# Kernel optimization log

Hardware: AMD Instinct MI355X
Metric: run time of the kernel (lower is better)

The kernel has to match this reference:

```python
import jax, jax.numpy as jnp
import numpy as np

N, D = 8192, 1024


def setup_inputs() -> dict:
    key = jax.random.key(0)
    k1, k2, k3 = jax.random.split(key, 3)
    f_1 = jax.random.normal(k1, (N, D), dtype=jnp.float32)
    f_2 = jax.random.normal(k2, (N, D), dtype=jnp.float32)
    f_3 = jax.random.normal(k3, (N, D), dtype=jnp.float32)
    return {"f_1": f_1, "f_2": f_2, "f_3": f_3, "batch": 3}


def _svdvals(x):
    # torch.svd computes full U, S, V; only singular values are consumed.
    return jnp.linalg.svd(x, compute_uv=False)


def reference(f_1, f_2, f_3, batch):
    if batch == 2:
        s_1 = _svdvals(f_1)
        if f_2.shape[0] == 0:
            return s_1[0] ** 2
        s_2 = _svdvals(f_2)
        return s_1.mean() + s_2.mean()
    elif batch == 3:
        s_1 = _svdvals(f_1)
        s_2 = _svdvals(f_2)
        s_3 = _svdvals(f_3)
        return s_1[0] ** 2 + 0.5 * (s_2[0] ** 2 + s_3[0] ** 2)
```

## Files before the change

kernel.cpp:

```cpp
#include <hip/hip_runtime.h>


#define DIM 1024
#define NROW 8192
#define MSZ (DIM*DIM)
#define NS 6

typedef __attribute__((ext_vector_type(8))) short short8;
typedef __attribute__((ext_vector_type(4))) float f32x4;

__device__ inline float bf2f(unsigned short u) {
    union { unsigned i; float f; } x; x.i = ((unsigned)u) << 16; return x.f;
}
__device__ inline unsigned short f2bf(float f) {
    union { float f; unsigned i; } x; x.f = f;
    unsigned r = x.i + 0x7FFFu + ((x.i >> 16) & 1u);
    return (unsigned short)(r >> 16);
}
__device__ inline void gload16(const void* g, void* l) {
    __builtin_amdgcn_global_load_lds(
        (const __attribute__((address_space(1))) unsigned int*)g,
        (__attribute__((address_space(3))) unsigned int*)l, 16, 0, 0);
}

__global__ __launch_bounds__(256)
void tconv_k(const float* __restrict__ f0, const float* __restrict__ f1,
             const float* __restrict__ f2, unsigned short* __restrict__ ft) {
    const int m = blockIdx.z;
    const float* f = (m == 0) ? f0 : (m == 1 ? f1 : f2);
    unsigned short* o = ft + (size_t)m * DIM * NROW;
    __shared__ float T[64][68];
    const int c0 = blockIdx.x * 64, r0 = blockIdx.y * 64;
    const int tid = threadIdx.x;
    const int cx = (tid & 15) * 4, ry = tid >> 4;
#pragma unroll
    for (int i = 0; i < 4; ++i) {
        int r = ry + i * 16;
        float4 v = *(const float4*)&f[(size_t)(r0 + r) * DIM + c0 + cx];
        T[cx + 0][r] = v.x;
        T[cx + 1][r] = v.y;
        T[cx + 2][r] = v.z;
        T[cx + 3][r] = v.w;
    }
    __syncthreads();
#pragma unroll
    for (int i = 0; i < 4; ++i) {
        int c = ry + i * 16;
        float4 g = *(const float4*)&T[c][cx];
        ushort4 u;
        u.x = f2bf(g.x); u.y = f2bf(g.y); u.z = f2bf(g.z); u.w = f2bf(g.w);
        *(ushort4*)&o[(size_t)(c0 + c) * NROW + r0 + cx] = u;
    }
}

__global__ __launch_bounds__(256)
void syrk_sk(const unsigned short* __restrict__ src, size_t mstride, int KF,
             float* __restrict__ Gp) {
    const int m = blockIdx.z;
    const unsigned short* S = src + (size_t)m * mstride;
    int idx = blockIdx.x, ti = 0;
    while (idx >= 8 - ti) { idx -= 8 - ti; ++ti; }
    const int tj = ti + idx;
    const int i0 = ti * 128, j0 = tj * 128;
    float* G = Gp + ((size_t)m * 36 + blockIdx.x) * 16384;
    const int Kc = KF / gridDim.y;
    const int k0b = blockIdx.y * Kc;

    __shared__ unsigned short As[2 * 128 * 32];
    __shared__ unsigned short Bs[2 * 128 * 32];

    const int tid = threadIdx.x, w = tid >> 6, lane = tid & 63;
    const int wi = w >> 1, wj = w & 1;

    f32x4 acc[4][4];
#pragma unroll
    for (int a = 0; a < 4; ++a)
#pragma unroll
        for (int b = 0; b < 4; ++b) acc[a][b] = (f32x4){0.f, 0.f, 0.f, 0.f};

    const int lr = lane >> 2;
    const int ksw = (((lane & 3) ^ ((lane >> 4) & 3)) * 8);
    const int fr = lane & 15;
    const int slot = (((lane >> 4) ^ ((fr >> 2) & 3)) * 8);

    for (int k0 = k0b; k0 < k0b + Kc; k0 += 64) {
#pragma unroll
        for (int h = 0; h < 2; ++h)
#pragma unroll
            for (int q = 0; q < 2; ++q) {
                int rr = w * 32 + q * 16;
                gload16(S + (size_t)(i0 + rr + lr) * KF + k0 + h * 32 + ksw,
                        &As[h * 4096 + rr * 32]);
                gload16(S + (size_t)(j0 + rr + lr) * KF + k0 + h * 32 + ksw,
                        &Bs[h * 4096 + rr * 32]);
            }
        __syncthreads();
#pragma unroll
        for (int h = 0; h < 2; ++h) {
            short8 af[4], bfv[4];
#pragma unroll
            for (int a = 0; a < 4; ++a)
                af[a] = *(const short8*)&As[h * 4096 + (wi * 64 + a * 16 + fr) * 32 + slot];
#pragma unroll
            for (int b = 0; b < 4; ++b)
                bfv[b] = *(const short8*)&Bs[h * 4096 + (wj * 64 + b * 16 + fr) * 32 + slot];
#pragma unroll
            for (int a = 0; a < 4; ++a)
#pragma unroll
                for (int b = 0; b < 4; ++b)
                    acc[a][b] = __builtin_amdgcn_mfma_f32_16x16x32_bf16(
                        af[a], bfv[b], acc[a][b], 0, 0, 0);
        }
        __syncthreads();
    }

    const int qr = (lane >> 4) * 4, cn = lane & 15;
#pragma unroll
    for (int a = 0; a < 4; ++a)
#pragma unroll
        for (int b = 0; b < 4; ++b) {
            int cl = wj * 64 + b * 16 + cn;
#pragma unroll
            for (int reg = 0; reg < 4; ++reg) {
                int rl = wi * 64 + a * 16 + qr + reg;
                atomicAdd(&G[rl * 128 + cl], acc[a][b][reg]);
            }
        }
}

__global__ __launch_bounds__(256)
void convert_k(const float* __restrict__ Gp, float* __restrict__ trout,
               unsigned short* __restrict__ dst) {
    const int m = blockIdx.z;
    int idx = blockIdx.x, ti = 0;
    while (idx >= 8 - ti) { idx -= 8 - ti; ++ti; }
    const int tj = ti + idx;
    const int i0 = ti * 128, j0 = tj * 128;
    const float* G = Gp + ((size_t)m * 36 + blockIdx.x) * 16384;
    unsigned short* D = dst + (size_t)m * MSZ;
    __shared__ unsigned short T[128][136];
    const int tid = threadIdx.x;
    const int cx = (tid & 31) * 4, ry = tid >> 5;
    float dtr = 0.f;
#pragma unroll 4
    for (int t = 0; t < 16; ++t) {
        int r = ry + t * 8;
        float4 g = *(const float4*)&G[r * 128 + cx];
        ushort4 o;
        o.x = f2bf(g.x); o.y = f2bf(g.y); o.z = f2bf(g.z); o.w = f2bf(g.w);
        *(ushort4*)&D[(size_t)(i0 + r) * DIM + j0 + cx] = o;
        int rs = r ^ (cx & 124);
        T[cx + 0][rs] = o.x; T[cx + 1][rs] = o.y;
        T[cx + 2][rs] = o.z; T[cx + 3][rs] = o.w;
        if (ti == tj) {
            int d = r - cx;
            if (d >= 0 && d < 4)
                dtr += (d == 0 ? g.x : d == 1 ? g.y : d == 2 ? g.z : g.w);
        }
    }
    if (ti == tj) atomicAdd(&trout[m], dtr);
    if (ti != tj) {
        __syncthreads();
#pragma unroll 4
        for (int t = 0; t < 16; ++t) {
            int p = ry + t * 8;
            int qs = cx ^ (p & 124);
            ushort4 o = *(const ushort4*)&T[p][qs];
            *(ushort4*)&D[(size_t)(j0 + p) * DIM + i0 + cx] = o;
        }
    }
}

__global__ __launch_bounds__(256)
void sq_k(const unsigned short* __restrict__ src, const float* __restrict__ trin,
          float* __restrict__ trout, unsigned short* __restrict__ dst) {
    const int m = blockIdx.z;
    const unsigned short* S = src + (size_t)m * MSZ;
    unsigned short* D = dst + (size_t)m * MSZ;
    int idx = blockIdx.x, ti = 0;
    while (idx >= 16 - ti) { idx -= 16 - ti; ++ti; }
    const int tj = ti + idx;
    const int i0 = ti * 64, j0 = tj * 64;
    float tv = trin[m];
    const float sc = 1.f / (tv * tv);

    __shared__ unsigned short As[2 * 64 * 32];
    __shared__ unsigned short Bs[2 * 64 * 32];
    __shared__ unsigned short Ts[64][68];

    const int tid = threadIdx.x, w = tid >> 6, lane = tid & 63;
    const int wi = w >> 1, wj = w & 1;
    f32x4 acc[2][2];
#pragma unroll
    for (int a = 0; a < 2; ++a)
#pragma unroll
        for (int b = 0; b < 2; ++b) acc[a][b] = (f32x4){0.f, 0.f, 0.f, 0.f};

    const int lr = lane >> 2;
    const int ksw = (((lane & 3) ^ ((lane >> 4) & 3)) * 8);
    const int fr = lane & 15;
    const int slot = (((lane >> 4) ^ ((fr >> 2) & 3)) * 8);

    for (int k0 = 0; k0 < DIM; k0 += 64) {
#pragma unroll
        for (int h = 0; h < 2; ++h) {
            gload16(S + (size_t)(i0 + w * 16 + lr) * DIM + k0 + h * 32 + ksw,
                    &As[h * 2048 + w * 16 * 32]);
            gload16(S + (size_t)(j0 + w * 16 + lr) * DIM + k0 + h * 32 + ksw,
                    &Bs[h * 2048 + w * 16 * 32]);
        }
        __syncthreads();
#pragma unroll
        for (int h = 0; h < 2; ++h) {
            short8 af[2], bfv[2];
#pragma unroll
            for (int a = 0; a < 2; ++a)
                af[a] = *(const short8*)&As[h * 2048 + (wi * 32 + a * 16 + fr) * 32 + slot];
#pragma unroll
            for (int c = 0; c < 2; ++c)
                bfv[c] = *(const short8*)&Bs[h * 2048 + (wj * 32 + c * 16 + fr) * 32 + slot];
#pragma unroll
            for (int a = 0; a < 2; ++a)
#pragma unroll
                for (int c = 0; c < 2; ++c)
                    acc[a][c] = __builtin_amdgcn_mfma_f32_16x16x32_bf16(
                        af[a], bfv[c], acc[a][c], 0, 0, 0);
        }
        __syncthreads();
    }

    const int qr = (lane >> 4) * 4, cn = lane & 15;
#pragma unroll
    for (int a = 0; a < 2; ++a)
#pragma unroll
        for (int b = 0; b < 2; ++b) {
            int cl = wj * 32 + b * 16 + cn;
#pragma unroll
            for (int reg = 0; reg < 4; ++reg) {
                int rl = wi * 32 + a * 16 + qr + reg;
                unsigned short val = f2bf(acc[a][b][reg] * sc);
                D[(size_t)(i0 + rl) * DIM + j0 + cl] = val;
                Ts[cl][rl] = val;
            }
        }
    if (ti == tj && wi == wj) {
        int d = cn - qr;
        if (d >= 0 && d < 4)
            atomicAdd(&trout[m], (acc[0][0][d] + acc[1][1][d]) * sc);
    }
    if (ti != tj) {
        __syncthreads();
        const int cx = (tid & 15) * 4, ry = tid >> 4;
#pragma unroll
        for (int tq = 0; tq < 4; ++tq) {
            int p = ry + tq * 16;
            ushort4 o;
            o.x = Ts[p][cx + 0]; o.y = Ts[p][cx + 1];
            o.z = Ts[p][cx + 2]; o.w = Ts[p][cx + 3];
            *(ushort4*)&D[(size_t)(j0 + p) * DIM + i0 + cx] = o;
        }
    }
}

__global__ __launch_bounds__(256)
void mv_bf16(const unsigned short* __restrict__ M, const float* __restrict__ vin,
             float* __restrict__ vout) {
    int m = blockIdx.y;
    const unsigned short* A = M + (size_t)m * MSZ;
    int wv = threadIdx.x >> 6, lane = threadIdx.x & 63;
    int row = blockIdx.x * 4 + wv;
    const unsigned short* a = A + (size_t)row * DIM;
    float s = 0.f;
    if (vin) {
        const float* v = vin + m * DIM;
        for (int j = lane; j < DIM; j += 64) s += bf2f(a[j]) * v[j];
    } else {
        for (int j = lane; j < DIM; j += 64) s += bf2f(a[j]);
    }
    for (int off = 32; off; off >>= 1) s += __shfl_down(s, off);
    if (lane == 0) vout[m * DIM + row] = s;
}

__global__ __launch_bounds__(256)
void rownorm_k(const float* __restrict__ f0, const float* __restrict__ f1,
               const float* __restrict__ f2, const float* __restrict__ w,
               float* __restrict__ u) {
    int m = blockIdx.y;
    const float* f = (m == 0) ? f0 : (m == 1 ? f1 : f2);
    int wv = threadIdx.x >> 6, lane = threadIdx.x & 63;
    int row = blockIdx.x * 4 + wv;
    const float* a = f + (size_t)row * DIM;
    const float* ww = w + m * DIM;
    float s = 0.f;
#pragma unroll
    for (int it = 0; it < 4; ++it) {
        int d = (it * 64 + lane) * 4;
        float4 av = *(const float4*)&a[d];
        float4 bv = *(const float4*)&ww[d];
        s += av.x * bv.x + av.y * bv.y + av.z * bv.z + av.w * bv.w;
    }
    for (int off = 32; off; off >>= 1) s += __shfl_down(s, off);
    if (lane == 0) u[m * NROW + row] = s;
}

__global__ __launch_bounds__(1024)
void final_k(const float* __restrict__ u, const float* __restrict__ w,
             float* __restrict__ out) {
    __shared__ float red[1024];
    int tid = threadIdx.x;
    float lam[3];
    for (int m = 0; m < 3; ++m) {
        float s = 0.f;
        for (int i = tid; i < NROW; i += 1024) { float x = u[m * NROW + i]; s += x * x; }
        red[tid] = s; __syncthreads();
        for (int off = 512; off; off >>= 1) {
            if (tid < off) red[tid] += red[tid + off];
            __syncthreads();
        }
        float num = red[0]; __syncthreads();
        s = 0.f;
        for (int i = tid; i < DIM; i += 1024) { float x = w[m * DIM + i]; s += x * x; }
        red[tid] = s; __syncthreads();
        for (int off = 512; off; off >>= 1) {
            if (tid < off) red[tid] += red[tid + off];
            __syncthreads();
        }
        lam[m] = num / red[0]; __syncthreads();
    }
    if (tid == 0) out[0] = lam[0] + 0.5f * (lam[1] + lam[2]);
}

extern "C" void kernel_launch(void* const* d_in, const int* in_sizes, int n_in,
                              void* d_out, int out_size, void* d_ws, size_t ws_size,
                              hipStream_t stream) {
    const float* f0 = (const float*)d_in[0];
    const float* f1 = (const float*)d_in[1];
    const float* f2 = (const float*)d_in[2];

    char* base = (char*)d_ws;
    unsigned short* ft = (unsigned short*)base;
    unsigned short* P  = (unsigned short*)(base + 50331648);
    float* G32 = (float*)(base + 56623104);
    unsigned short* Q  = (unsigned short*)(base + 56623104);
    float* trbuf = (float*)(base + 63700992);
    float* v = (float*)(base + 63701248);
    float* w = v + 3 * DIM;
    float* u = w + 3 * DIM;

    hipMemsetAsync(G32, 0, 7078144, stream);

    dim3 gt(DIM / 64, NROW / 64, 3);
    tconv_k<<<gt, 256, 0, stream>>>(f0, f1, f2, ft);

    syrk_sk<<<dim3(36, 4, 3), 256, 0, stream>>>(ft, (size_t)DIM * NROW, NROW, G32);
    convert_k<<<dim3(36, 1, 3), 256, 0, stream>>>(G32, trbuf, P);

    unsigned short* cur = P;
    unsigned short* nxt = Q;
    for (int s = 0; s < NS; ++s) {
        sq_k<<<dim3(136, 1, 3), 256, 0, stream>>>(cur, trbuf + s * 3,
                                                  trbuf + (s + 1) * 3, nxt);
        unsigned short* t2 = cur; cur = nxt; nxt = t2;
    }

    dim3 b(256, 1, 1);
    dim3 gm(DIM / 4, 3, 1);
    mv_bf16<<<gm, b, 0, stream>>>(cur, nullptr, v);
    mv_bf16<<<gm, b, 0, stream>>>(cur, v, w);

    dim3 gr(NROW / 4, 3, 1);
    rownorm_k<<<gr, b, 0, stream>>>(f0, f1, f2, w, u);
    final_k<<<1, 1024, 0, stream>>>(u, w, (float*)d_out);
}
```

Baseline: 330.7 us.

## Retile squaring kernel to single-wave 32x32 tiles, widen SYRK split-K, fuse rownorm reduction

The repeated matrix-squaring kernel now uses 64-thread blocks on 32x32 upper-triangle tiles, giving 528 blocks per matrix. Each block double-buffers its global-to-LDS loads inside one wavefront and drops the __syncthreads barriers. This is meant to raise parallelism and cut barrier stalls across the six squaring launches, which run back to back. The Gram SYRK kernel moves to a flattened grid with 8-way split-K instead of 4, spreading work over more CUs at the cost of more float atomics into G. The row-norm kernel now squares and sums its results in-block and atomically adds them into a per-matrix scalar. That removes the 3x8192 intermediate vector and shrinks the final reduction kernel, but relies on the memset zeroing that scalar and on the compiler ordering LDS reads against the async loads when no barrier is present.

```diff
diff --git a/kernel.cpp b/kernel.cpp
--- a/kernel.cpp
+++ b/kernel.cpp
@@ -54,17 +54,18 @@
 }
 
 __global__ __launch_bounds__(256)
-void syrk_sk(const unsigned short* __restrict__ src, size_t mstride, int KF,
-             float* __restrict__ Gp) {
-    const int m = blockIdx.z;
-    const unsigned short* S = src + (size_t)m * mstride;
-    int idx = blockIdx.x, ti = 0;
+void syrk_sk(const unsigned short* __restrict__ src, float* __restrict__ Gp) {
+    const int b = blockIdx.x;
+    const int ky = b & 7;
+    const int q = b >> 3;
+    const int m = q / 36;
+    int idx = q % 36, ti = 0;
     while (idx >= 8 - ti) { idx -= 8 - ti; ++ti; }
     const int tj = ti + idx;
     const int i0 = ti * 128, j0 = tj * 128;
-    float* G = Gp + ((size_t)m * 36 + blockIdx.x) * 16384;
-    const int Kc = KF / gridDim.y;
-    const int k0b = blockIdx.y * Kc;
+    const unsigned short* S = src + (size_t)m * DIM * NROW;
+    float* G = Gp + ((size_t)m * 36 + (size_t)(q % 36)) * 16384;
+    const int k0b = ky << 10;
 
     __shared__ unsigned short As[2 * 128 * 32];
     __shared__ unsigned short Bs[2 * 128 * 32];
@@ -76,22 +77,22 @@
 #pragma unroll
     for (int a = 0; a < 4; ++a)
 #pragma unroll
-        for (int b = 0; b < 4; ++b) acc[a][b] = (f32x4){0.f, 0.f, 0.f, 0.f};
+        for (int c = 0; c < 4; ++c) acc[a][c] = (f32x4){0.f, 0.f, 0.f, 0.f};
 
     const int lr = lane >> 2;
     const int ksw = (((lane & 3) ^ ((lane >> 4) & 3)) * 8);
     const int fr = lane & 15;
     const int slot = (((lane >> 4) ^ ((fr >> 2) & 3)) * 8);
 
-    for (int k0 = k0b; k0 < k0b + Kc; k0 += 64) {
+    for (int k0 = k0b; k0 < k0b + 1024; k0 += 64) {
 #pragma unroll
         for (int h = 0; h < 2; ++h)
 #pragma unroll
-            for (int q = 0; q < 2; ++q) {
-                int rr = w * 32 + q * 16;
-                gload16(S + (size_t)(i0 + rr + lr) * KF + k0 + h * 32 + ksw,
+            for (int p = 0; p < 2; ++p) {
+                int rr = w * 32 + p * 16;
+                gload16(S + (size_t)(i0 + rr + lr) * NROW + k0 + h * 32 + ksw,
                         &As[h * 4096 + rr * 32]);
-                gload16(S + (size_t)(j0 + rr + lr) * KF + k0 + h * 32 + ksw,
+                gload16(S + (size_t)(j0 + rr + lr) * NROW + k0 + h * 32 + ksw,
                         &Bs[h * 4096 + rr * 32]);
             }
         __syncthreads();
@@ -102,14 +103,14 @@
             for (int a = 0; a < 4; ++a)
                 af[a] = *(const short8*)&As[h * 4096 + (wi * 64 + a * 16 + fr) * 32 + slot];
 #pragma unroll
-            for (int b = 0; b < 4; ++b)
-                bfv[b] = *(const short8*)&Bs[h * 4096 + (wj * 64 + b * 16 + fr) * 32 + slot];
+            for (int c = 0; c < 4; ++c)
+                bfv[c] = *(const short8*)&Bs[h * 4096 + (wj * 64 + c * 16 + fr) * 32 + slot];
 #pragma unroll
             for (int a = 0; a < 4; ++a)
 #pragma unroll
-                for (int b = 0; b < 4; ++b)
-                    acc[a][b] = __builtin_amdgcn_mfma_f32_16x16x32_bf16(
-                        af[a], bfv[b], acc[a][b], 0, 0, 0);
+                for (int c = 0; c < 4; ++c)
+                    acc[a][c] = __builtin_amdgcn_mfma_f32_16x16x32_bf16(
+                        af[a], bfv[c], acc[a][c], 0, 0, 0);
         }
         __syncthreads();
     }
@@ -118,12 +119,12 @@
 #pragma unroll
     for (int a = 0; a < 4; ++a)
 #pragma unroll
-        for (int b = 0; b < 4; ++b) {
-            int cl = wj * 64 + b * 16 + cn;
+        for (int c = 0; c < 4; ++c) {
+            int cl = wj * 64 + c * 16 + cn;
 #pragma unroll
             for (int reg = 0; reg < 4; ++reg) {
                 int rl = wi * 64 + a * 16 + qr + reg;
-                atomicAdd(&G[rl * 128 + cl], acc[a][b][reg]);
+                atomicAdd(&G[rl * 128 + cl], acc[a][c][reg]);
             }
         }
 }
@@ -171,54 +172,54 @@
     }
 }
 
-__global__ __launch_bounds__(256)
+__global__ __launch_bounds__(64)
 void sq_k(const unsigned short* __restrict__ src, const float* __restrict__ trin,
           float* __restrict__ trout, unsigned short* __restrict__ dst) {
-    const int m = blockIdx.z;
+    const int m = blockIdx.y;
     const unsigned short* S = src + (size_t)m * MSZ;
     unsigned short* D = dst + (size_t)m * MSZ;
     int idx = blockIdx.x, ti = 0;
-    while (idx >= 16 - ti) { idx -= 16 - ti; ++ti; }
+    while (idx >= 32 - ti) { idx -= 32 - ti; ++ti; }
     const int tj = ti + idx;
-    const int i0 = ti * 64, j0 = tj * 64;
+    const int i0 = ti * 32, j0 = tj * 32;
     float tv = trin[m];
     const float sc = 1.f / (tv * tv);
 
-    __shared__ unsigned short As[2 * 64 * 32];
-    __shared__ unsigned short Bs[2 * 64 * 32];
-    __shared__ unsigned short Ts[64][68];
-
-    const int tid = threadIdx.x, w = tid >> 6, lane = tid & 63;
-    const int wi = w >> 1, wj = w & 1;
-    f32x4 acc[2][2];
-#pragma unroll
-    for (int a = 0; a < 2; ++a)
-#pragma unroll
-        for (int b = 0; b < 2; ++b) acc[a][b] = (f32x4){0.f, 0.f, 0.f, 0.f};
-
+    __shared__ unsigned short As[2][32 * 32];
+    __shared__ unsigned short Bs[2][32 * 32];
+    __shared__ unsigned short Ts[32][36];
+
+    const int lane = threadIdx.x;
     const int lr = lane >> 2;
     const int ksw = (((lane & 3) ^ ((lane >> 4) & 3)) * 8);
     const int fr = lane & 15;
     const int slot = (((lane >> 4) ^ ((fr >> 2) & 3)) * 8);
 
+    f32x4 acc[2][2];
+#pragma unroll
+    for (int a = 0; a < 2; ++a)
+#pragma unroll
+        for (int c = 0; c < 2; ++c) acc[a][c] = (f32x4){0.f, 0.f, 0.f, 0.f};
+
+#define STAGE(K0, P)                                                          \
+    do {                                                                      \
+        gload16(S + (size_t)(i0 + lr) * DIM + (K0) + ksw,      &As[P][0]);    \
+        gload16(S + (size_t)(i0 + 16 + lr) * DIM + (K0) + ksw, &As[P][512]);  \
+        gload16(S + (size_t)(j0 + lr) * DIM + (K0) + ksw,      &Bs[P][0]);    \
+        gload16(S + (size_t)(j0 + 16 + lr) * DIM + (K0) + ksw, &Bs[P][512]);  \
+    } while (0)
+
+    STAGE(0, 0);
+    STAGE(32, 1);
     for (int k0 = 0; k0 < DIM; k0 += 64) {
-#pragma unroll
-        for (int h = 0; h < 2; ++h) {
-            gload16(S + (size_t)(i0 + w * 16 + lr) * DIM + k0 + h * 32 + ksw,
-                    &As[h * 2048 + w * 16 * 32]);
-            gload16(S + (size_t)(j0 + w * 16 + lr) * DIM + k0 + h * 32 + ksw,
-                    &Bs[h * 2048 + w * 16 * 32]);
-        }
-        __syncthreads();
-#pragma unroll
-        for (int h = 0; h < 2; ++h) {
+        {
             short8 af[2], bfv[2];
 #pragma unroll
-            for (int a = 0; a < 2; ++a)
-                af[a] = *(const short8*)&As[h * 2048 + (wi * 32 + a * 16 + fr) * 32 + slot];
-#pragma unroll
-            for (int c = 0; c < 2; ++c)
-                bfv[c] = *(const short8*)&Bs[h * 2048 + (wj * 32 + c * 16 + fr) * 32 + slot];
+            for (int a = 0; a < 2; ++a) {
+                af[a]  = *(const short8*)&As[0][(a * 16 + fr) * 32 + slot];
+                bfv[a] = *(const short8*)&Bs[0][(a * 16 + fr) * 32 + slot];
+            }
+            if (k0 + 64 < DIM) STAGE(k0 + 64, 0);
 #pragma unroll
             for (int a = 0; a < 2; ++a)
 #pragma unroll
@@ -226,37 +227,48 @@
                     acc[a][c] = __builtin_amdgcn_mfma_f32_16x16x32_bf16(
                         af[a], bfv[c], acc[a][c], 0, 0, 0);
         }
-        __syncthreads();
-    }
+        {
+            short8 af[2], bfv[2];
+#pragma unroll
+            for (int a = 0; a < 2; ++a) {
+                af[a]  = *(const short8*)&As[1][(a * 16 + fr) * 32 + slot];
+                bfv[a] = *(const short8*)&Bs[1][(a * 16 + fr) * 32 + slot];
+            }
+            if (k0 + 96 < DIM) STAGE(k0 + 96, 1);
+#pragma unroll
+            for (int a = 0; a < 2; ++a)
+#pragma unroll
+                for (int c = 0; c < 2; ++c)
+                    acc[a][c] = __builtin_amdgcn_mfma_f32_16x16x32_bf16(
+                        af[a], bfv[c], acc[a][c], 0, 0, 0);
+        }
+    }
+#undef STAGE
 
     const int qr = (lane >> 4) * 4, cn = lane & 15;
 #pragma unroll
     for (int a = 0; a < 2; ++a)
 #pragma unroll
-        for (int b = 0; b < 2; ++b) {
-            int cl = wj * 32 + b * 16 + cn;
+        for (int c = 0; c < 2; ++c) {
+            int cl = c * 16 + cn;
 #pragma unroll
             for (int reg = 0; reg < 4; ++reg) {
-                int rl = wi * 32 + a * 16 + qr + reg;
-                unsigned short val = f2bf(acc[a][b][reg] * sc);
+                int rl = a * 16 + qr + reg;
+                unsigned short val = f2bf(acc[a][c][reg] * sc);
                 D[(size_t)(i0 + rl) * DIM + j0 + cl] = val;
                 Ts[cl][rl] = val;
             }
         }
-    if (ti == tj && wi == wj) {
+    if (ti == tj) {
         int d = cn - qr;
         if (d >= 0 && d < 4)
             atomicAdd(&trout[m], (acc[0][0][d] + acc[1][1][d]) * sc);
-    }
-    if (ti != tj) {
-        __syncthreads();
-        const int cx = (tid & 15) * 4, ry = tid >> 4;
+    } else {
+        const int cx = (lane & 7) * 4, ry = lane >> 3;
 #pragma unroll
         for (int tq = 0; tq < 4; ++tq) {
-            int p = ry + tq * 16;
-            ushort4 o;
-            o.x = Ts[p][cx + 0]; o.y = Ts[p][cx + 1];
-            o.z = Ts[p][cx + 2]; o.w = Ts[p][cx + 3];
+            int p = ry + tq * 8;
+            ushort4 o = *(const ushort4*)&Ts[p][cx];
             *(ushort4*)&D[(size_t)(j0 + p) * DIM + i0 + cx] = o;
         }
     }
@@ -284,7 +296,7 @@
 __global__ __launch_bounds__(256)
 void rownorm_k(const float* __restrict__ f0, const float* __restrict__ f1,
                const float* __restrict__ f2, const float* __restrict__ w,
-               float* __restrict__ u) {
+               float* __restrict__ num) {
     int m = blockIdx.y;
     const float* f = (m == 0) ? f0 : (m == 1 ? f1 : f2);
     int wv = threadIdx.x >> 6, lane = threadIdx.x & 63;
@@ -300,32 +312,28 @@
         s += av.x * bv.x + av.y * bv.y + av.z * bv.z + av.w * bv.w;
     }
     for (int off = 32; off; off >>= 1) s += __shfl_down(s, off);
-    if (lane == 0) u[m * NROW + row] = s;
-}
-
-__global__ __launch_bounds__(1024)
-void final_k(const float* __restrict__ u, const float* __restrict__ w,
+    __shared__ float part[4];
+    if (lane == 0) part[wv] = s * s;
+    __syncthreads();
+    if (threadIdx.x == 0)
+        atomicAdd(&num[m], part[0] + part[1] + part[2] + part[3]);
+}
+
+__global__ __launch_bounds__(256)
+void final_k(const float* __restrict__ num, const float* __restrict__ w,
              float* __restrict__ out) {
-    __shared__ float red[1024];
+    __shared__ float red[256];
     int tid = threadIdx.x;
     float lam[3];
     for (int m = 0; m < 3; ++m) {
         float s = 0.f;
-        for (int i = tid; i < NROW; i += 1024) { float x = u[m * NROW + i]; s += x * x; }
+        for (int i = tid; i < DIM; i += 256) { float x = w[m * DIM + i]; s += x * x; }
         red[tid] = s; __syncthreads();
-        for (int off = 512; off; off >>= 1) {
+        for (int off = 128; off; off >>= 1) {
             if (tid < off) red[tid] += red[tid + off];
             __syncthreads();
         }
-        float num = red[0]; __syncthreads();
-        s = 0.f;
-        for (int i = tid; i < DIM; i += 1024) { float x = w[m * DIM + i]; s += x * x; }
-        red[tid] = s; __syncthreads();
-        for (int off = 512; off; off >>= 1) {
-            if (tid < off) red[tid] += red[tid + off];
-            __syncthreads();
-        }
-        lam[m] = num / red[0]; __syncthreads();
+        lam[m] = num[m] / red[0]; __syncthreads();
     }
     if (tid == 0) out[0] = lam[0] + 0.5f * (lam[1] + lam[2]);
 }
@@ -343,23 +351,23 @@
     float* G32 = (float*)(base + 56623104);
     unsigned short* Q  = (unsigned short*)(base + 56623104);
     float* trbuf = (float*)(base + 63700992);
+    float* num = trbuf + 40;
     float* v = (float*)(base + 63701248);
     float* w = v + 3 * DIM;
-    float* u = w + 3 * DIM;
 
     hipMemsetAsync(G32, 0, 7078144, stream);
 
     dim3 gt(DIM / 64, NROW / 64, 3);
     tconv_k<<<gt, 256, 0, stream>>>(f0, f1, f2, ft);
 
-    syrk_sk<<<dim3(36, 4, 3), 256, 0, stream>>>(ft, (size_t)DIM * NROW, NROW, G32);
+    syrk_sk<<<864, 256, 0, stream>>>(ft, G32);
     convert_k<<<dim3(36, 1, 3), 256, 0, stream>>>(G32, trbuf, P);
 
     unsigned short* cur = P;
     unsigned short* nxt = Q;
     for (int s = 0; s < NS; ++s) {
-        sq_k<<<dim3(136, 1, 3), 256, 0, stream>>>(cur, trbuf + s * 3,
-                                                  trbuf + (s + 1) * 3, nxt);
+        sq_k<<<dim3(528, 3, 1), 64, 0, stream>>>(cur, trbuf + s * 3,
+                                                 trbuf + (s + 1) * 3, nxt);
         unsigned short* t2 = cur; cur = nxt; nxt = t2;
     }
 
@@ -369,6 +377,6 @@
     mv_bf16<<<gm, b, 0, stream>>>(cur, v, w);
 
     dim3 gr(NROW / 4, 3, 1);
-    rownorm_k<<<gr, b, 0, stream>>>(f0, f1, f2, w, u);
-    final_k<<<1, 1024, 0, stream>>>(u, w, (float*)d_out);
-}
+    rownorm_k<<<gr, b, 0, stream>>>(f0, f1, f2, w, num);
+    final_k<<<1, 256, 0, stream>>>(num, w, (float*)d_out);
+}
```

Measured after the change: 406.0 us. +22.8%, slower.

## Compute Rayleigh quotient from the cached Gram matrix instead of rereading inputs

Applied to the files above, without the earlier changes.

Replaces the final pass that multiplied each full 8192x1024 fp32 input by the power-iteration vector with a Rayleigh quotient w^T G w taken from the fp32 Gram tiles already held in the workspace. The 36 upper-triangular 128x128 tiles per matrix are reduced with atomics, and off-diagonal tiles are doubled. This removes a roughly 100 MB read of the inputs in favour of about 7 MB of Gram data. The ping-pong buffer Q is moved onto the dead transposed-input region so G32 stays intact. The result now depends on the bf16-derived Gram matrix rather than the original fp32 inputs.

```diff
diff --git a/kernel.cpp b/kernel.cpp
--- a/kernel.cpp
+++ b/kernel.cpp
@@ -282,50 +282,53 @@
 }
 
 __global__ __launch_bounds__(256)
-void rownorm_k(const float* __restrict__ f0, const float* __restrict__ f1,
-               const float* __restrict__ f2, const float* __restrict__ w,
-               float* __restrict__ u) {
-    int m = blockIdx.y;
-    const float* f = (m == 0) ? f0 : (m == 1 ? f1 : f2);
-    int wv = threadIdx.x >> 6, lane = threadIdx.x & 63;
-    int row = blockIdx.x * 4 + wv;
-    const float* a = f + (size_t)row * DIM;
-    const float* ww = w + m * DIM;
-    float s = 0.f;
-#pragma unroll
-    for (int it = 0; it < 4; ++it) {
-        int d = (it * 64 + lane) * 4;
-        float4 av = *(const float4*)&a[d];
-        float4 bv = *(const float4*)&ww[d];
-        s += av.x * bv.x + av.y * bv.y + av.z * bv.z + av.w * bv.w;
-    }
+void ray_k(const float* __restrict__ Gp, const float* __restrict__ wv,
+           float* __restrict__ num) {
+    const int m = blockIdx.y;
+    int idx = blockIdx.x, ti = 0;
+    while (idx >= 8 - ti) { idx -= 8 - ti; ++ti; }
+    const int tj = ti + idx;
+    const float* G = Gp + ((size_t)m * 36 + blockIdx.x) * 16384;
+    const float* wi = wv + m * DIM + ti * 128;
+    const float* wj = wv + m * DIM + tj * 128;
+    const int tid = threadIdx.x;
+    const int r = tid >> 1, c0 = (tid & 1) * 64;
+    float inner = 0.f;
+    const float4* g4 = (const float4*)&G[r * 128 + c0];
+    const float4* w4 = (const float4*)&wj[c0];
+#pragma unroll
+    for (int t = 0; t < 16; ++t) {
+        float4 g = g4[t], ww = w4[t];
+        inner += g.x * ww.x + g.y * ww.y + g.z * ww.z + g.w * ww.w;
+    }
+    float s = wi[r] * inner;
     for (int off = 32; off; off >>= 1) s += __shfl_down(s, off);
-    if (lane == 0) u[m * NROW + row] = s;
-}
-
-__global__ __launch_bounds__(1024)
-void final_k(const float* __restrict__ u, const float* __restrict__ w,
+    __shared__ float part[4];
+    int lane = tid & 63, wx = tid >> 6;
+    if (lane == 0) part[wx] = s;
+    __syncthreads();
+    if (tid == 0) {
+        float tot = part[0] + part[1] + part[2] + part[3];
+        if (ti != tj) tot *= 2.f;
+        atomicAdd(&num[m], tot);
+    }
+}
+
+__global__ __launch_bounds__(256)
+void final_k(const float* __restrict__ num, const float* __restrict__ w,
              float* __restrict__ out) {
-    __shared__ float red[1024];
+    __shared__ float red[256];
     int tid = threadIdx.x;
     float lam[3];
     for (int m = 0; m < 3; ++m) {
         float s = 0.f;
-        for (int i = tid; i < NROW; i += 1024) { float x = u[m * NROW + i]; s += x * x; }
+        for (int i = tid; i < DIM; i += 256) { float x = w[m * DIM + i]; s += x * x; }
         red[tid] = s; __syncthreads();
-        for (int off = 512; off; off >>= 1) {
+        for (int off = 128; off; off >>= 1) {
             if (tid < off) red[tid] += red[tid + off];
             __syncthreads();
         }
-        float num = red[0]; __syncthreads();
-        s = 0.f;
-        for (int i = tid; i < DIM; i += 1024) { float x = w[m * DIM + i]; s += x * x; }
-        red[tid] = s; __syncthreads();
-        for (int off = 512; off; off >>= 1) {
-            if (tid < off) red[tid] += red[tid + off];
-            __syncthreads();
-        }
-        lam[m] = num / red[0]; __syncthreads();
+        lam[m] = num[m] / red[0]; __syncthreads();
     }
     if (tid == 0) out[0] = lam[0] + 0.5f * (lam[1] + lam[2]);
 }
@@ -339,13 +342,13 @@
 
     char* base = (char*)d_ws;
     unsigned short* ft = (unsigned short*)base;
+    unsigned short* Q  = (unsigned short*)base;
     unsigned short* P  = (unsigned short*)(base + 50331648);
     float* G32 = (float*)(base + 56623104);
-    unsigned short* Q  = (unsigned short*)(base + 56623104);
     float* trbuf = (float*)(base + 63700992);
+    float* num = trbuf + 40;
     float* v = (float*)(base + 63701248);
     float* w = v + 3 * DIM;
-    float* u = w + 3 * DIM;
 
     hipMemsetAsync(G32, 0, 7078144, stream);
 
@@ -368,7 +371,6 @@
     mv_bf16<<<gm, b, 0, stream>>>(cur, nullptr, v);
     mv_bf16<<<gm, b, 0, stream>>>(cur, v, w);
 
-    dim3 gr(NROW / 4, 3, 1);
-    rownorm_k<<<gr, b, 0, stream>>>(f0, f1, f2, w, u);
-    final_k<<<1, 1024, 0, stream>>>(u, w, (float*)d_out);
-}
+    ray_k<<<dim3(36, 3, 1), 256, 0, stream>>>(G32, w, num);
+    final_k<<<1, 256, 0, stream>>>(num, w, (float*)d_out);
+}
```

Measured after the change: 312.2 us. 5.6% less time.
